# Kernel tuning notes

Hardware: AMD Instinct MI355X
Metric: run time of the kernel (lower is better)

Reference implementation:

```python
import itertools
import jax, jax.numpy as jnp
import numpy as np

B, N, D = 128, 1024, 256
G, GSZ, REL_DIM, KD, PD, NF = 64, 3, 16, 64, 64, 64


def sinusoidal_pe(n, d):
    # standard transformer sinusoidal positional encoding, shape (n, d)
    pos = jnp.arange(n, dtype=jnp.float32)[:, None]
    i = jnp.arange(d, dtype=jnp.float32)[None, :]
    angle = pos / jnp.power(10000.0, (2.0 * jnp.floor(i / 2.0)) / d)
    return jnp.where(jnp.arange(d)[None, :] % 2 == 0, jnp.sin(angle), jnp.cos(angle))


def setup_inputs() -> dict:
    key = jax.random.key(0)
    k0, k1, k2, k3, k4, k5 = jax.random.split(key, 6)
    x = jax.random.normal(k0, (B, N, D), jnp.float32)
    # graphlet filter bank (random_normal init)
    filters = 0.05 * jax.random.normal(k1, (NF, GSZ, GSZ, REL_DIM), jnp.float32)
    # learned group queries: Embedding(n_groups*graphlet_size, key_dim)
    query_emb = 0.05 * jax.random.normal(k2, (G * GSZ, KD), jnp.float32)
    # Dense(key_dim, use_bias=False) for attention keys
    Wk_map = jax.random.normal(k3, (D, KD), jnp.float32) / np.sqrt(D)
    # MultiDimInnerProdRelation: per-relation-dim query/key projections
    Wq = jax.random.normal(k4, (REL_DIM, D, PD), jnp.float32) / np.sqrt(D)
    Wk = jax.random.normal(k5, (REL_DIM, D, PD), jnp.float32) / np.sqrt(D)
    return {"x": x, "filters": filters, "query_emb": query_emb,
            "Wk_map": Wk_map, "Wq": Wq, "Wk": Wk}


def reference(x, filters, query_emb, Wk_map, Wq, Wk):
    beta = KD ** (-0.5)
    # group attention: keys = Dense(x) + positional embedding ('pos+feat')
    k = jnp.einsum('bnd,dk->bnk', x, Wk_map) + sinusoidal_pe(N, KD)[None]
    scores = jax.nn.softmax(beta * jnp.einsum('qk,bnk->bqn', query_emb, k), axis=-1)
    gobj = jnp.einsum('bqn,bnd->bqd', scores, x).reshape(B, G, GSZ, D)
    # MultiDimInnerProdRelation within each group: R[b,g,i,j,r] = <Wq_r x_i, Wk_r x_j>
    zq = jnp.einsum('bgnd,rdp->bgrnp', gobj, Wq)
    zk = jnp.einsum('bgmd,rdp->bgrmp', gobj, Wk)
    R = jnp.einsum('bgrnp,bgrmp->bgnmr', zq, zk)  # (B, G, GSZ, GSZ, REL_DIM)
    # symmetric relational inner product: aggregate (mean) over permutations
    perms = jnp.array(list(itertools.permutations(range(GSZ))))  # (P, GSZ)
    Rp = R[:, :, perms[:, :, None], perms[:, None, :], :]  # (B, G, P, GSZ, GSZ, REL_DIM)
    ip = jnp.einsum('bgpnmr,fnmr->bgpf', Rp, filters)
    return jnp.mean(ip, axis=2)  # (B, n_groups, n_filters)
```

## Files before the change

kernel.cpp:

```cpp
#include <hip/hip_runtime.h>
#include <math.h>

#define B_   128
#define N_   1024
#define D_   256
#define G_   64
#define GSZ_ 3
#define RD_  16
#define KD_  64
#define PD_  64
#define NF_  64
#define Q_   (G_*GSZ_)

typedef __attribute__((ext_vector_type(8))) short bf16x8;
typedef __attribute__((ext_vector_type(4))) float f32x4;

__device__ __forceinline__ unsigned short f2bf(float f) {
    unsigned int u = __float_as_uint(f);
    u += 0x7fffu + ((u >> 16) & 1u);
    return (unsigned short)(u >> 16);
}

__global__ void coef_kernel(const float* __restrict__ filters,
                            float* __restrict__ coef) {
    int flat = blockIdx.x * 256 + threadIdx.x;
    if (flat >= NF_ * RD_) return;
    int f = flat >> 4, r = flat & 15;
    const float* F = filters + f * 144 + r;
    float diag = F[0] + F[48 + 16] + F[96 + 32];
    float all = 0.f;
#pragma unroll
    for (int u = 0; u < 3; ++u)
#pragma unroll
        for (int v = 0; v < 3; ++v) all += F[u * 48 + v * 16];
    float a = diag * (1.f / 3.f);
    float b = (all - diag) * (1.f / 6.f);
    coef[f * 16 + r] = a - b;
    coef[1024 + f * 16 + r] = b;
}

__global__ __launch_bounds__(256)
void wb2_kernel(const float* __restrict__ Wq,
                const float* __restrict__ Wk,
                unsigned short* __restrict__ Wb) {
    __shared__ unsigned short wt[64 * 264];
    int qk = blockIdx.x >> 4, r = blockIdx.x & 15;
    const float* W = qk ? Wk : Wq;
    int t = threadIdx.x;
#pragma unroll
    for (int i = 0; i < 16; ++i) {
        int flat = i * 256 + t;
        int d = flat >> 4, p4 = flat & 15;
        float4 v = *(const float4*)(W + ((size_t)r * 256 + d) * 64 + p4 * 4);
        wt[(p4 * 4 + 0) * 264 + d] = f2bf(v.x);
        wt[(p4 * 4 + 1) * 264 + d] = f2bf(v.y);
        wt[(p4 * 4 + 2) * 264 + d] = f2bf(v.z);
        wt[(p4 * 4 + 3) * 264 + d] = f2bf(v.w);
    }
    __syncthreads();
    size_t base = (size_t)(qk * 16 + r) * 16384;
#pragma unroll
    for (int i = 0; i < 8; ++i) {
        int flat = i * 256 + t;
        int p = flat >> 5, seg = flat & 31;
        *(uint4*)(Wb + base + (size_t)(seg >> 2) * 2048 + p * 32 + (seg & 3) * 8) =
            *(const uint4*)(&wt[p * 264 + seg * 8]);
    }
}

__global__ void qeb_kernel(const float* __restrict__ qe,
                           unsigned short* __restrict__ qeb) {
    int i = blockIdx.x * 256 + threadIdx.x;
    if (i < Q_ * KD_) qeb[i] = f2bf(qe[i] * 0.125f);
}

__global__ void wkt_kernel(const float* __restrict__ Wk_map,
                           unsigned short* __restrict__ WkTb) {
    int i = blockIdx.x * 256 + threadIdx.x;
    int kd = i >> 8, d = i & 255;
    WkTb[kd * 256 + d] = f2bf(Wk_map[d * 64 + kd]);
}

#define WKP 264

__global__ __launch_bounds__(256, 2)
void xkp_kernel(const float* __restrict__ x,
                const unsigned short* __restrict__ WkTb,
                unsigned short* __restrict__ kbf,
                unsigned short* __restrict__ xtf) {
    __shared__ unsigned short wkts[64 * WKP];
    __shared__ unsigned short xs[64 * WKP];
    __shared__ unsigned short Ks[64 * 72];
    int b = blockIdx.y, n0 = blockIdx.x * 64;
    int t = threadIdx.x, w = t >> 6, lane = t & 63;
    int quad = lane >> 4, lcol = lane & 15;

#pragma unroll
    for (int i = 0; i < 8; ++i) {
        int f = i * 256 + t;
        int row = f >> 5, seg = f & 31;
        *(uint4*)(&wkts[row * WKP + seg * 8]) = *(const uint4*)(WkTb + row * 256 + seg * 8);
    }
#pragma unroll
    for (int i = 0; i < 16; ++i) {
        int f = i * 256 + t;
        int row = f >> 6, c4 = f & 63;
        float4 v = *(const float4*)(x + ((size_t)b * N_ + n0 + row) * D_ + c4 * 4);
        uint2 uv;
        uv.x = (unsigned int)f2bf(v.x) | ((unsigned int)f2bf(v.y) << 16);
        uv.y = (unsigned int)f2bf(v.z) | ((unsigned int)f2bf(v.w) << 16);
        *(uint2*)(&xs[row * WKP + c4 * 4]) = uv;
    }
    __syncthreads();

    f32x4 z[4];
#pragma unroll
    for (int mt = 0; mt < 4; ++mt) z[mt] = (f32x4)(0.f);
#pragma unroll
    for (int kk = 0; kk < 8; ++kk) {
        bf16x8 bf = *(const bf16x8*)(&xs[(w * 16 + lcol) * WKP + kk * 32 + quad * 8]);
#pragma unroll
        for (int mt = 0; mt < 4; ++mt) {
            bf16x8 af = *(const bf16x8*)(&wkts[(mt * 16 + lcol) * WKP + kk * 32 + quad * 8]);
            z[mt] = __builtin_amdgcn_mfma_f32_16x16x32_bf16(af, bf, z[mt], 0, 0, 0);
        }
    }

    int nl = w * 16 + lcol;
    int n = n0 + nl;
#pragma unroll
    for (int mt = 0; mt < 4; ++mt)
#pragma unroll
        for (int r = 0; r < 4; ++r) {
            int kd = mt * 16 + quad * 4 + r;
            float freq  = expf(-(float)(kd >> 1) * (logf(10000.0f) / 32.0f));
            float angle = (float)n * freq;
            float pe    = (kd & 1) ? cosf(angle) : sinf(angle);
            Ks[nl * 72 + kd] = f2bf(z[mt][r] + pe);
        }

    {
        int dt = t >> 4, lc = t & 15;
        int c = blockIdx.x >> 1;
        int ks0 = (blockIdx.x & 1) * 2;
#pragma unroll
        for (int i = 0; i < 8; ++i) {
            uint4 uv; unsigned short* us = (unsigned short*)&uv;
#pragma unroll
            for (int e = 0; e < 8; ++e)
                us[e] = xs[(i * 8 + e) * WKP + t];
            *(uint4*)(xtf + ((((size_t)b * 16 + dt) * 8 + c) * 4 + ks0 + (i >> 2)) * 512
                            + (size_t)lc * 32 + (i & 3) * 8) = uv;
        }
    }
    __syncthreads();

#pragma unroll
    for (int i = 0; i < 2; ++i) {
        int f = i * 256 + t;
        int row = f >> 3, seg = f & 7;
        int ntile = (n0 >> 4) + (row >> 4), lc = row & 15;
        int ks = seg >> 2, quad8 = (seg & 3) * 8;
        *(uint4*)(kbf + ((size_t)(b * 64 + ntile) * 2 + ks) * 512 + lc * 32 + quad8) =
            *(const uint4*)(&Ks[row * 72 + seg * 8]);
    }
}

#define PSP2 136

__global__ __launch_bounds__(512, 2)
void attn5_kernel(const unsigned short* __restrict__ qeb,
                  const unsigned short* __restrict__ kbf,
                  const unsigned short* __restrict__ xtf,
                  unsigned short* __restrict__ gobj) {
    __shared__ unsigned short ps[96 * PSP2];
    __shared__ float Rs[96][8];
    __shared__ float invs[96];

    int b = blockIdx.x >> 1, qh = blockIdx.x & 1;
    int t = threadIdx.x, w = t >> 6, lane = t & 63;
    int quad = lane >> 4, lcol = lane & 15;
    int q0 = qh * 96;

    bf16x8 qef[6][2];
#pragma unroll
    for (int mt = 0; mt < 6; ++mt)
#pragma unroll
        for (int ks = 0; ks < 2; ++ks)
            qef[mt][ks] = *(const bf16x8*)(qeb + (q0 + mt * 16 + lcol) * KD_ + ks * 32 + quad * 8);

    f32x4 acc[2][6];
#pragma unroll
    for (int i = 0; i < 2; ++i)
#pragma unroll
        for (int mt = 0; mt < 6; ++mt) acc[i][mt] = (f32x4)(0.f);
    float rsum[6][4];
#pragma unroll
    for (int mt = 0; mt < 6; ++mt)
#pragma unroll
        for (int r = 0; r < 4; ++r) rsum[mt][r] = 0.f;

    const unsigned short* kbB = kbf + (size_t)b * 65536;
    const unsigned short* xtB = xtf + (size_t)b * 262144;

    for (int c = 0; c < 8; ++c) {
        f32x4 s[6];
#pragma unroll
        for (int mt = 0; mt < 6; ++mt) s[mt] = (f32x4)(0.f);
#pragma unroll
        for (int ks = 0; ks < 2; ++ks) {
            bf16x8 bf = *(const bf16x8*)(kbB + (size_t)((c * 8 + w) * 2 + ks) * 512 + lcol * 32 + quad * 8);
#pragma unroll
            for (int mt = 0; mt < 6; ++mt)
                s[mt] = __builtin_amdgcn_mfma_f32_16x16x32_bf16(qef[mt][ks], bf, s[mt], 0, 0, 0);
        }
#pragma unroll
        for (int mt = 0; mt < 6; ++mt)
#pragma unroll
            for (int r = 0; r < 4; ++r) {
                float e = __expf(s[mt][r]);
                s[mt][r] = e;
                rsum[mt][r] += e;
            }
        __syncthreads();
#pragma unroll
        for (int mt = 0; mt < 6; ++mt)
#pragma unroll
            for (int r = 0; r < 4; ++r)
                ps[(mt * 16 + quad * 4 + r) * PSP2 + w * 16 + lcol] = f2bf(s[mt][r]);
        __syncthreads();

#pragma unroll
        for (int ks = 0; ks < 4; ++ks) {
            bf16x8 af[6];
#pragma unroll
            for (int mt = 0; mt < 6; ++mt)
                af[mt] = *(const bf16x8*)(ps + (mt * 16 + lcol) * PSP2 + ks * 32 + quad * 8);
#pragma unroll
            for (int i = 0; i < 2; ++i) {
                int dt = i * 8 + w;
                bf16x8 bf = *(const bf16x8*)(xtB + (size_t)(((dt * 8 + c) * 4 + ks) * 16 + lcol) * 32 + quad * 8);
#pragma unroll
                for (int mt = 0; mt < 6; ++mt)
                    acc[i][mt] = __builtin_amdgcn_mfma_f32_16x16x32_bf16(af[mt], bf, acc[i][mt], 0, 0, 0);
            }
        }
    }

#pragma unroll
    for (int mt = 0; mt < 6; ++mt)
#pragma unroll
        for (int r = 0; r < 4; ++r) {
            float v = rsum[mt][r];
            v += __shfl_xor(v, 1, 64);
            v += __shfl_xor(v, 2, 64);
            v += __shfl_xor(v, 4, 64);
            v += __shfl_xor(v, 8, 64);
            rsum[mt][r] = v;
        }
    if (lcol == 0) {
#pragma unroll
        for (int mt = 0; mt < 6; ++mt)
#pragma unroll
            for (int r = 0; r < 4; ++r)
                Rs[mt * 16 + quad * 4 + r][w] = rsum[mt][r];
    }
    __syncthreads();
    if (t < 96) {
        float s8 = 0.f;
#pragma unroll
        for (int ww = 0; ww < 8; ++ww) s8 += Rs[t][ww];
        invs[t] = 1.0f / s8;
    }
    __syncthreads();

    unsigned short* gB = gobj + ((size_t)b * Q_ + q0) * D_;
#pragma unroll
    for (int i = 0; i < 2; ++i) {
        int dt = i * 8 + w;
#pragma unroll
        for (int mt = 0; mt < 6; ++mt)
#pragma unroll
            for (int r = 0; r < 4; ++r) {
                int q = mt * 16 + quad * 4 + r;
                gB[q * D_ + dt * 16 + lcol] = f2bf(acc[i][mt][r] * invs[q]);
            }
    }
}

#define AP4 264

__global__ __launch_bounds__(512, 2)
void rel10_kernel(const unsigned short* __restrict__ gobj,
                  const unsigned short* __restrict__ Wb,
                  const float* __restrict__ coef,
                  float* __restrict__ out) {
    __shared__ unsigned short As[64 * AP4];
    __shared__ float Tp[2048];

    int t = threadIdx.x, w = t >> 6, lane = t & 63;
    int quad = lane >> 4, lcol = lane & 15;
    int pgrp = w & 3, rh = w >> 2;
    int bg0 = blockIdx.x * 16;
    int pcol = pgrp * 16 + lcol;

    {
        int r3 = t >> 5, c4 = t & 31;
        uint4 zz; zz.x = zz.y = zz.z = zz.w = 0u;
        *(uint4*)(&As[(r3 * 4 + 3) * AP4 + c4 * 8]) = zz;
    }
#pragma unroll
    for (int i = 0; i < 3; ++i) {
        int idx = i * 512 + t;
        int j = idx >> 5, c4 = idx & 31;
        *(uint4*)(&As[((j / 3) * 4 + (j % 3)) * AP4 + c4 * 8]) =
            *(const uint4*)(gobj + ((size_t)(bg0 * 3 + j)) * 256 + c4 * 8);
    }
    __syncthreads();

    for (int r8 = 0; r8 < 8; ++r8) {
        int r = rh * 8 + r8;
        f32x4 zq[4], zk[4];
#pragma unroll
        for (int mt = 0; mt < 4; ++mt) { zq[mt] = (f32x4)(0.f); zk[mt] = (f32x4)(0.f); }
        const unsigned short* bqp = Wb + (size_t)r * 16384 + pcol * 32 + quad * 8;
        const unsigned short* bkp = bqp + (size_t)262144;
#pragma unroll
        for (int kk = 0; kk < 8; ++kk) {
            bf16x8 bq = *(const bf16x8*)(bqp + kk * 2048);
            bf16x8 bk = *(const bf16x8*)(bkp + kk * 2048);
#pragma unroll
            for (int mt = 0; mt < 4; ++mt) {
                bf16x8 a_ = *(const bf16x8*)(&As[(mt * 16 + lcol) * AP4 + kk * 32 + quad * 8]);
                zq[mt] = __builtin_amdgcn_mfma_f32_16x16x32_bf16(a_, bq, zq[mt], 0, 0, 0);
                zk[mt] = __builtin_amdgcn_mfma_f32_16x16x32_bf16(a_, bk, zk[mt], 0, 0, 0);
            }
        }
#pragma unroll
        for (int mt = 0; mt < 4; ++mt) {
            float t1 = zq[mt].x * zk[mt].x + zq[mt].y * zk[mt].y +
                       zq[mt].z * zk[mt].z + zq[mt].w * zk[mt].w;
            float sq = zq[mt].x + zq[mt].y + zq[mt].z + zq[mt].w;
            float sk = zk[mt].x + zk[mt].y + zk[mt].z + zk[mt].w;
            float t2 = sq * sk;
#pragma unroll
            for (int off = 1; off < 16; off <<= 1) {
                t1 += __shfl_xor(t1, off, 64);
                t2 += __shfl_xor(t2, off, 64);
            }
            if (lcol == 0) {
                int bgl = mt * 4 + quad;
                Tp[((pgrp * 16 + bgl) * 2 + 0) * 16 + r] = t1;
                Tp[((pgrp * 16 + bgl) * 2 + 1) * 16 + r] = t2;
            }
        }
    }
    __syncthreads();

    int f = t & 63, grp = t >> 6;
#pragma unroll
    for (int i = 0; i < 2; ++i) {
        int bgl = grp * 2 + i;
        float a = 0.f;
#pragma unroll
        for (int r = 0; r < 16; ++r) {
            float T1 = Tp[((0 * 16 + bgl) * 2 + 0) * 16 + r] + Tp[((1 * 16 + bgl) * 2 + 0) * 16 + r] +
                       Tp[((2 * 16 + bgl) * 2 + 0) * 16 + r] + Tp[((3 * 16 + bgl) * 2 + 0) * 16 + r];
            float T2 = Tp[((0 * 16 + bgl) * 2 + 1) * 16 + r] + Tp[((1 * 16 + bgl) * 2 + 1) * 16 + r] +
                       Tp[((2 * 16 + bgl) * 2 + 1) * 16 + r] + Tp[((3 * 16 + bgl) * 2 + 1) * 16 + r];
            a += coef[f * 16 + r] * T1 + coef[1024 + f * 16 + r] * T2;
        }
        out[(size_t)(bg0 + bgl) * NF_ + f] = a;
    }
}

extern "C" void kernel_launch(void* const* d_in, const int* in_sizes, int n_in,
                              void* d_out, int out_size, void* d_ws, size_t ws_size,
                              hipStream_t stream) {
    const float* x         = (const float*)d_in[0];
    const float* filters   = (const float*)d_in[1];
    const float* query_emb = (const float*)d_in[2];
    const float* Wk_map    = (const float*)d_in[3];
    const float* Wq        = (const float*)d_in[4];
    const float* Wk        = (const float*)d_in[5];
    float* out = (float*)d_out;

    char* p = (char*)d_ws;
    unsigned short* xtf  = (unsigned short*)p;  p += (size_t)B_*D_*N_*2;
    unsigned short* kbf  = (unsigned short*)p;  p += (size_t)B_*N_*KD_*2;
    unsigned short* gobj = (unsigned short*)p;  p += (size_t)B_*Q_*D_*2;
    unsigned short* Wb   = (unsigned short*)p;  p += (size_t)2048*256*2;
    float*          coef = (float*)p;           p += 2048*4;
    unsigned short* qeb  = (unsigned short*)p;  p += (size_t)Q_*KD_*2;
    unsigned short* WkTb = (unsigned short*)p;  p += (size_t)KD_*D_*2;

    hipLaunchKernelGGL(wkt_kernel, dim3(64), dim3(256), 0, stream,
                       Wk_map, WkTb);
    hipLaunchKernelGGL(qeb_kernel, dim3(48), dim3(256), 0, stream,
                       query_emb, qeb);
    hipLaunchKernelGGL(coef_kernel, dim3(4), dim3(256), 0, stream,
                       filters, coef);
    hipLaunchKernelGGL(wb2_kernel, dim3(32), dim3(256), 0, stream,
                       Wq, Wk, Wb);
    hipLaunchKernelGGL(xkp_kernel, dim3(16, 128), dim3(256), 0, stream,
                       x, WkTb, kbf, xtf);
    hipLaunchKernelGGL(attn5_kernel, dim3(256), dim3(512), 0, stream,
                       qeb, kbf, xtf, gobj);
    hipLaunchKernelGGL(rel10_kernel, dim3(512), dim3(512), 0, stream,
                       gobj, Wb, coef, out);
}
```

Baseline: 333.9 us.

## Precompute positional encoding table and read pre-swizzled key weights from global

The sinusoidal positional encoding is now precomputed once into a fragment-ordered float table, which seeds the MFMA accumulators, so the per-element expf/sinf/cosf work in xkp_kernel goes away. The key-map weights are stored pre-swizzled in MFMA fragment order and read directly from global/L2 instead of being staged in shared memory. That frees LDS and the launch bound is raised to three blocks per SM, with the kk loop unroll reduced to 2. The cost is an extra launch, a 256KB pe table read by every block, and global-latency weight loads inside the MFMA loop.

```diff
diff --git a/kernel.cpp b/kernel.cpp
--- a/kernel.cpp
+++ b/kernel.cpp
@@ -75,32 +75,38 @@
 }
 
 __global__ void wkt_kernel(const float* __restrict__ Wk_map,
-                           unsigned short* __restrict__ WkTb) {
+                           unsigned short* __restrict__ WkTbf) {
     int i = blockIdx.x * 256 + threadIdx.x;
-    int kd = i >> 8, d = i & 255;
-    WkTb[kd * 256 + d] = f2bf(Wk_map[d * 64 + kd]);
+    int e = i & 7, quad = (i >> 3) & 3, lcol = (i >> 5) & 15;
+    int kk = (i >> 9) & 7, mt = (i >> 12) & 3;
+    int kd = mt * 16 + lcol, d = kk * 32 + quad * 8 + e;
+    WkTbf[i] = f2bf(Wk_map[d * 64 + kd]);
+}
+
+__global__ void pef_kernel(float* __restrict__ pef) {
+    int i = blockIdx.x * 256 + threadIdx.x;
+    int r = i & 3, lane = (i >> 2) & 63, mt = (i >> 8) & 3, ntile = i >> 10;
+    int n = ntile * 16 + (lane & 15);
+    int kd = mt * 16 + (lane >> 4) * 4 + r;
+    float freq  = expf(-(float)(kd >> 1) * (logf(10000.0f) / 32.0f));
+    float angle = (float)n * freq;
+    pef[i] = (kd & 1) ? cosf(angle) : sinf(angle);
 }
 
 #define WKP 264
 
-__global__ __launch_bounds__(256, 2)
+__global__ __launch_bounds__(256, 3)
 void xkp_kernel(const float* __restrict__ x,
-                const unsigned short* __restrict__ WkTb,
+                const unsigned short* __restrict__ WkTbf,
+                const float* __restrict__ pef,
                 unsigned short* __restrict__ kbf,
                 unsigned short* __restrict__ xtf) {
-    __shared__ unsigned short wkts[64 * WKP];
     __shared__ unsigned short xs[64 * WKP];
     __shared__ unsigned short Ks[64 * 72];
     int b = blockIdx.y, n0 = blockIdx.x * 64;
     int t = threadIdx.x, w = t >> 6, lane = t & 63;
     int quad = lane >> 4, lcol = lane & 15;
 
-#pragma unroll
-    for (int i = 0; i < 8; ++i) {
-        int f = i * 256 + t;
-        int row = f >> 5, seg = f & 31;
-        *(uint4*)(&wkts[row * WKP + seg * 8]) = *(const uint4*)(WkTb + row * 256 + seg * 8);
-    }
 #pragma unroll
     for (int i = 0; i < 16; ++i) {
         int f = i * 256 + t;
@@ -115,29 +121,24 @@
 
     f32x4 z[4];
 #pragma unroll
-    for (int mt = 0; mt < 4; ++mt) z[mt] = (f32x4)(0.f);
-#pragma unroll
+    for (int mt = 0; mt < 4; ++mt)
+        z[mt] = *(const f32x4*)(pef + (((size_t)(blockIdx.x * 4 + w) * 4 + mt) * 64 + lane) * 4);
+#pragma unroll 2
     for (int kk = 0; kk < 8; ++kk) {
         bf16x8 bf = *(const bf16x8*)(&xs[(w * 16 + lcol) * WKP + kk * 32 + quad * 8]);
 #pragma unroll
         for (int mt = 0; mt < 4; ++mt) {
-            bf16x8 af = *(const bf16x8*)(&wkts[(mt * 16 + lcol) * WKP + kk * 32 + quad * 8]);
+            bf16x8 af = *(const bf16x8*)(WkTbf + ((mt * 8 + kk) << 9) + lcol * 32 + quad * 8);
             z[mt] = __builtin_amdgcn_mfma_f32_16x16x32_bf16(af, bf, z[mt], 0, 0, 0);
         }
     }
 
     int nl = w * 16 + lcol;
-    int n = n0 + nl;
 #pragma unroll
     for (int mt = 0; mt < 4; ++mt)
 #pragma unroll
-        for (int r = 0; r < 4; ++r) {
-            int kd = mt * 16 + quad * 4 + r;
-            float freq  = expf(-(float)(kd >> 1) * (logf(10000.0f) / 32.0f));
-            float angle = (float)n * freq;
-            float pe    = (kd & 1) ? cosf(angle) : sinf(angle);
-            Ks[nl * 72 + kd] = f2bf(z[mt][r] + pe);
-        }
+        for (int r = 0; r < 4; ++r)
+            Ks[nl * 72 + mt * 16 + quad * 4 + r] = f2bf(z[mt][r]);
 
     {
         int dt = t >> 4, lc = t & 15;
@@ -386,16 +387,19 @@
     float* out = (float*)d_out;
 
     char* p = (char*)d_ws;
-    unsigned short* xtf  = (unsigned short*)p;  p += (size_t)B_*D_*N_*2;
-    unsigned short* kbf  = (unsigned short*)p;  p += (size_t)B_*N_*KD_*2;
-    unsigned short* gobj = (unsigned short*)p;  p += (size_t)B_*Q_*D_*2;
-    unsigned short* Wb   = (unsigned short*)p;  p += (size_t)2048*256*2;
-    float*          coef = (float*)p;           p += 2048*4;
-    unsigned short* qeb  = (unsigned short*)p;  p += (size_t)Q_*KD_*2;
-    unsigned short* WkTb = (unsigned short*)p;  p += (size_t)KD_*D_*2;
+    unsigned short* xtf   = (unsigned short*)p;  p += (size_t)B_*D_*N_*2;
+    unsigned short* kbf   = (unsigned short*)p;  p += (size_t)B_*N_*KD_*2;
+    unsigned short* gobj  = (unsigned short*)p;  p += (size_t)B_*Q_*D_*2;
+    unsigned short* Wb    = (unsigned short*)p;  p += (size_t)2048*256*2;
+    float*          coef  = (float*)p;           p += 2048*4;
+    unsigned short* qeb   = (unsigned short*)p;  p += (size_t)Q_*KD_*2;
+    unsigned short* WkTbf = (unsigned short*)p;  p += (size_t)KD_*D_*2;
+    float*          pef   = (float*)p;           p += (size_t)65536*4;
 
     hipLaunchKernelGGL(wkt_kernel, dim3(64), dim3(256), 0, stream,
-                       Wk_map, WkTb);
+                       Wk_map, WkTbf);
+    hipLaunchKernelGGL(pef_kernel, dim3(256), dim3(256), 0, stream,
+                       pef);
     hipLaunchKernelGGL(qeb_kernel, dim3(48), dim3(256), 0, stream,
                        query_emb, qeb);
     hipLaunchKernelGGL(coef_kernel, dim3(4), dim3(256), 0, stream,
@@ -403,7 +407,7 @@
     hipLaunchKernelGGL(wb2_kernel, dim3(32), dim3(256), 0, stream,
                        Wq, Wk, Wb);
     hipLaunchKernelGGL(xkp_kernel, dim3(16, 128), dim3(256), 0, stream,
-                       x, WkTb, kbf, xtf);
+                       x, WkTbf, pef, kbf, xtf);
     hipLaunchKernelGGL(attn5_kernel, dim3(256), dim3(512), 0, stream,
                        qeb, kbf, xtf, gobj);
     hipLaunchKernelGGL(rel10_kernel, dim3(512), dim3(512), 0, stream,
```

New measurement: 343.0 us. 1.03x slower.
